# Kernel tuning notes

Hardware: AMD Instinct MI355X
Metric: run time of the kernel (lower is better)

Reference implementation:

```python
import jax, jax.numpy as jnp
import numpy as np

SHAPES = [(100, 100), (50, 50), (25, 25), (13, 13)]
N_HEADS, N_LEVELS, N_POINTS, D_MODEL, D_FFN = 8, 4, 4, 256, 1024
HEAD_DIM = D_MODEL // N_HEADS
S_TOTAL = sum(h * w for h, w in SHAPES)
BATCH = 2


def _layernorm(x, g, b, eps=1e-5):
    m = jnp.mean(x, -1, keepdims=True)
    v = jnp.mean((x - m) ** 2, -1, keepdims=True)
    return (x - m) * jax.lax.rsqrt(v + eps) * g + b


def _bilinear_sample(value_l, loc, Hl, Wl):
    # value_l: (N, Hl, Wl, nh, hd); loc: (N, Lq, nh, P, 2) normalized to [0,1]
    # Matches torch grid_sample(mode='bilinear', padding_mode='zeros', align_corners=False)
    x = loc[..., 0] * Wl - 0.5
    y = loc[..., 1] * Hl - 0.5
    x0 = jnp.floor(x); y0 = jnp.floor(y)
    wx1 = x - x0; wx0 = 1.0 - wx1
    wy1 = y - y0; wy0 = 1.0 - wy1
    x0i = x0.astype(jnp.int32); x1i = x0i + 1
    y0i = y0.astype(jnp.int32); y1i = y0i + 1
    N, Lq, nh, P = x.shape
    n_idx = jnp.arange(N)[:, None, None, None]
    h_idx = jnp.arange(nh)[None, None, :, None]

    def gather(yi, xi):
        valid = (yi >= 0) & (yi < Hl) & (xi >= 0) & (xi < Wl)
        yc = jnp.clip(yi, 0, Hl - 1); xc = jnp.clip(xi, 0, Wl - 1)
        v = value_l[n_idx, yc, xc, h_idx]  # (N, Lq, nh, P, hd)
        return v * valid[..., None].astype(v.dtype)

    return (gather(y0i, x0i) * (wy0 * wx0)[..., None]
            + gather(y0i, x1i) * (wy0 * wx1)[..., None]
            + gather(y1i, x0i) * (wy1 * wx0)[..., None]
            + gather(y1i, x1i) * (wy1 * wx1)[..., None])


def _forward(src, pos, reference_points, W_off, b_off, W_attn, b_attn, W_val, b_val,
             W_out, b_out, W1, b1, W2, b2, g1, beta1, g2, beta2):
    N, S, C = src.shape
    q = src + pos  # with_pos_embed
    # MSDeformAttn
    off = (q @ W_off + b_off).reshape(N, S, N_HEADS, N_LEVELS, N_POINTS, 2)
    aw = jax.nn.softmax((q @ W_attn + b_attn).reshape(N, S, N_HEADS, N_LEVELS * N_POINTS), axis=-1)
    aw = aw.reshape(N, S, N_HEADS, N_LEVELS, N_POINTS)
    value = (src @ W_val + b_val).reshape(N, S, N_HEADS, HEAD_DIM)
    # offset normalizer is (W_l, H_l) per level
    normalizer = jnp.array([[wl, hl] for hl, wl in SHAPES], dtype=src.dtype)  # (L, 2)
    loc = reference_points[:, :, None, :, None, :] + off / normalizer[None, None, None, :, None, :]
    out = jnp.zeros((N, S, N_HEADS, HEAD_DIM), src.dtype)
    start = 0
    for l, (Hl, Wl) in enumerate(SHAPES):
        v_l = value[:, start:start + Hl * Wl].reshape(N, Hl, Wl, N_HEADS, HEAD_DIM)
        sampled = _bilinear_sample(v_l, loc[:, :, :, l], Hl, Wl)  # (N,S,nh,P,hd)
        out = out + jnp.einsum('nqhp,nqhpd->nqhd', aw[:, :, :, l], sampled)
        start += Hl * Wl
    src2 = out.reshape(N, S, C) @ W_out + b_out
    # residual + norm1 (dropout is identity in eval)
    x = _layernorm(src + src2, g1, beta1)
    # FFN + residual + norm2
    ff = jax.nn.relu(x @ W1 + b1) @ W2 + b2
    return _layernorm(x + ff, g2, beta2)


def setup_inputs() -> dict:
    key = jax.random.key(0)
    ks = jax.random.split(key, 16)
    f32 = jnp.float32

    def w(k, shape, scale=0.02):
        return jax.random.normal(k, shape, dtype=f32) * scale

    return {
        "src": jax.random.normal(ks[0], (BATCH, S_TOTAL, D_MODEL), dtype=f32),
        "pos": jax.random.normal(ks[1], (BATCH, S_TOTAL, D_MODEL), dtype=f32),
        "reference_points": jax.random.uniform(ks[2], (BATCH, S_TOTAL, N_LEVELS, 2), dtype=f32),
        "spatial_shapes": jnp.array(SHAPES, dtype=jnp.int32),
        "level_start_index": jnp.array(np.cumsum([0] + [h * w for h, w in SHAPES[:-1]]), dtype=jnp.int32),
        "W_off": w(ks[3], (D_MODEL, N_HEADS * N_LEVELS * N_POINTS * 2)),
        "b_off": w(ks[4], (N_HEADS * N_LEVELS * N_POINTS * 2,), 0.5),
        "W_attn": w(ks[5], (D_MODEL, N_HEADS * N_LEVELS * N_POINTS)),
        "b_attn": w(ks[6], (N_HEADS * N_LEVELS * N_POINTS,)),
        "W_val": w(ks[7], (D_MODEL, D_MODEL)),
        "b_val": w(ks[8], (D_MODEL,)),
        "W_out": w(ks[9], (D_MODEL, D_MODEL)),
        "b_out": w(ks[10], (D_MODEL,)),
        "W1": w(ks[11], (D_MODEL, D_FFN)),
        "b1": w(ks[12], (D_FFN,)),
        "W2": w(ks[13], (D_FFN, D_MODEL)),
        "b2": w(ks[14], (D_MODEL,)),
        "g1": jnp.ones((D_MODEL,), f32),
        "beta1": jnp.zeros((D_MODEL,), f32),
        "g2": jnp.ones((D_MODEL,), f32),
        "beta2": jnp.zeros((D_MODEL,), f32),
    }


def reference(src, pos, reference_points, spatial_shapes, level_start_index,
              W_off, b_off, W_attn, b_attn, W_val, b_val, W_out, b_out,
              W1, b1, W2, b2, g1, beta1, g2, beta2):
    # spatial_shapes / level_start_index are static metadata mirrored by SHAPES
    return _forward(src, pos, reference_points, W_off, b_off, W_attn, b_attn,
                    W_val, b_val, W_out, b_out, W1, b1, W2, b2, g1, beta1, g2, beta2)
```

## Files before the change

### kernel.cpp

```cpp
#include <hip/hip_runtime.h>


typedef __bf16 bf16x8 __attribute__((ext_vector_type(8)));
typedef __bf16 bf16x4 __attribute__((ext_vector_type(4)));
typedef float floatx4 __attribute__((ext_vector_type(4)));

#define S_TOTAL 13294
#define M_ROWS  26588
#define M_PAD   26624

#define MFMA16(a, b, c) __builtin_amdgcn_mfma_f32_16x16x32_bf16(a, b, c, 0, 0, 0)

__global__ __launch_bounds__(256) void cvt_k(
    const float* __restrict__ Woff, const float* __restrict__ Wattn,
    const float* __restrict__ Wval, const float* __restrict__ Wout,
    const float* __restrict__ W1,   const float* __restrict__ W2,
    const float* __restrict__ boff, const float* __restrict__ battn,
    __bf16* __restrict__ wbase, float* __restrict__ bc) {
    int b = blockIdx.x;
    if (b >= 184) {
        for (int i = threadIdx.x; i < 384; i += 256)
            bc[i] = (i < 256) ? boff[i] : battn[i - 256];
        return;
    }
    const float* W; __bf16* D; int K, N, t;
    if (b < 16)       { W = Woff;  D = wbase;          K = 256;  N = 256;  t = b; }
    else if (b < 24)  { W = Wattn; D = wbase + 65536;  K = 256;  N = 128;  t = b - 16; }
    else if (b < 40)  { W = Wval;  D = wbase + 98304;  K = 256;  N = 256;  t = b - 24; }
    else if (b < 56)  { W = Wout;  D = wbase + 163840; K = 256;  N = 256;  t = b - 40; }
    else if (b < 120) { W = W1;    D = wbase + 229376; K = 256;  N = 1024; t = b - 56; }
    else              { W = W2;    D = wbase + 491520; K = 1024; N = 256;  t = b - 120; }
    int tk = K >> 6;
    int n0 = (t / tk) << 6, k0 = (t % tk) << 6;
    __shared__ float T[64][65];
    int tid = threadIdx.x;
    int rr = tid >> 4, cc = (tid & 15) << 2;
#pragma unroll
    for (int p = 0; p < 4; p++) {
        int r = p * 16 + rr;
        float4 v = *(const float4*)(W + (size_t)(k0 + r) * N + n0 + cc);
        T[r][cc] = v.x; T[r][cc + 1] = v.y; T[r][cc + 2] = v.z; T[r][cc + 3] = v.w;
    }
    __syncthreads();
#pragma unroll
    for (int p = 0; p < 4; p++) {
        int n = p * 16 + rr;
        bf16x4 o = {(__bf16)T[cc][n], (__bf16)T[cc + 1][n],
                    (__bf16)T[cc + 2][n], (__bf16)T[cc + 3][n]};
        *(bf16x4*)(D + (size_t)(n0 + n) * K + k0 + cc) = o;
    }
}

template <int J, bool SUMPOS, bool BF16OUT>
__global__ __launch_bounds__(512, 4) void gemm_src(
    const float* __restrict__ Af, const float* __restrict__ Pf,
    const __bf16* __restrict__ BT, const float* __restrict__ bias,
    float* __restrict__ Cf, __bf16* __restrict__ Cb, int N) {
    constexpr int ASTR = 264;
    __shared__ __align__(16) __bf16 As[64 * ASTR];
    __shared__ __align__(16) float patch[8][16 * 20];
    const int tid = threadIdx.x, wave = tid >> 6, lane = tid & 63;
    const int l16 = lane & 15, quad = lane >> 4;
    const int row0 = blockIdx.x * 64;
#pragma unroll
    for (int p = 0; p < 8; p++) {
        int fe = (p * 512 + tid) * 4;
        int m = fe >> 8, k = fe & 255;
        int row = min(row0 + m, M_ROWS - 1);
        float4 s = *(const float4*)(Af + (size_t)row * 256 + k);
        if (SUMPOS) {
            float4 pp = *(const float4*)(Pf + (size_t)row * 256 + k);
            s.x += pp.x; s.y += pp.y; s.z += pp.z; s.w += pp.w;
        }
        bf16x4 v = {(__bf16)s.x, (__bf16)s.y, (__bf16)s.z, (__bf16)s.w};
        *(bf16x4*)(As + m * ASTR + k) = v;
    }
    __syncthreads();
    const int n0 = wave * (J * 16);
    floatx4 acc[4][J] = {};
#pragma unroll
    for (int ki = 0; ki < 8; ki++) {
        bf16x8 af[4], bfr[J];
#pragma unroll
        for (int i = 0; i < 4; i++)
            af[i] = *(const bf16x8*)(As + (i * 16 + l16) * ASTR + ki * 32 + quad * 8);
#pragma unroll
        for (int j = 0; j < J; j++)
            bfr[j] = *(const bf16x8*)(BT + (size_t)(n0 + j * 16 + l16) * 256 + ki * 32 + quad * 8);
#pragma unroll
        for (int i = 0; i < 4; i++)
#pragma unroll
            for (int j = 0; j < J; j++)
                acc[i][j] = MFMA16(af[i], bfr[j], acc[i][j]);
    }
    float* pat = patch[wave];
    const int prow = lane >> 2, pc = lane & 3;
#pragma unroll
    for (int i = 0; i < 4; i++)
#pragma unroll
        for (int j = 0; j < J; j++) {
            float bv = bias[n0 + j * 16 + l16];
#pragma unroll
            for (int r = 0; r < 4; r++)
                pat[(quad * 4 + r) * 20 + l16] = acc[i][j][r] + bv;
            float4 v4 = *(float4*)&pat[prow * 20 + pc * 4];
            size_t gi = (size_t)(row0 + i * 16 + prow) * N + n0 + j * 16 + pc * 4;
            if (BF16OUT) {
                bf16x4 ob = {(__bf16)v4.x, (__bf16)v4.y, (__bf16)v4.z, (__bf16)v4.w};
                *(bf16x4*)(Cb + gi) = ob;
            } else {
                *(float4*)(Cf + gi) = v4;
            }
        }
}

__global__ __launch_bounds__(256) void sample_k(const float* __restrict__ offa,
                                                const __bf16* __restrict__ valb,
                                                const float* __restrict__ refp,
                                                __bf16* __restrict__ outb) {
    const int r   = blockIdx.x;
    const int tid = threadIdx.x;
    if (r >= M_ROWS) {
        outb[(size_t)r * 256 + tid] = (__bf16)0.f;
        return;
    }
    __shared__ float2 s_wo[4][128];
    const int n = (r >= S_TOTAL) ? 1 : 0;

    if (tid < 128) {
        const int HLc[4] = {100, 50, 25, 13};
        const int STc[4] = {0, 10000, 12500, 13125};
        int lp = tid & 15, l = lp >> 2;
        float logit = offa[(size_t)r * 384 + 256 + tid];
        float mx = logit;
        mx = fmaxf(mx, __shfl_xor(mx, 1));
        mx = fmaxf(mx, __shfl_xor(mx, 2));
        mx = fmaxf(mx, __shfl_xor(mx, 4));
        mx = fmaxf(mx, __shfl_xor(mx, 8));
        float e = __expf(logit - mx);
        float s = e;
        s += __shfl_xor(s, 1); s += __shfl_xor(s, 2);
        s += __shfl_xor(s, 4); s += __shfl_xor(s, 8);
        float aw = e / s;

        float2 o2 = *(const float2*)(offa + (size_t)r * 384 + tid * 2);
        float rx = refp[((size_t)r * 4 + l) * 2];
        float ry = refp[((size_t)r * 4 + l) * 2 + 1];
        int   Wl = HLc[l];
        float x = rx * (float)Wl + o2.x - 0.5f;
        float y = ry * (float)Wl + o2.y - 0.5f;
        float xf = floorf(x), yf = floorf(y);
        float wx1 = x - xf, wy1 = y - yf;
        float wx0 = 1.f - wx1, wy0 = 1.f - wy1;
        int x0 = (int)xf, y0 = (int)yf;
        int base = n * S_TOTAL + STc[l];
#pragma unroll
        for (int c = 0; c < 4; c++) {
            int yy = y0 + (c >> 1), xx = x0 + (c & 1);
            bool valid = (yy >= 0) & (yy < Wl) & (xx >= 0) & (xx < Wl);
            int yc = min(max(yy, 0), Wl - 1);
            int xc = min(max(xx, 0), Wl - 1);
            float w = ((c >> 1) ? wy1 : wy0) * ((c & 1) ? wx1 : wx0);
            int off = (base + yc * Wl + xc) * 512;
            s_wo[c][tid] = make_float2(valid ? w * aw : 0.f, __int_as_float(off));
        }
    }
    __syncthreads();

    const int h  = tid >> 5;
    const int pg = (tid >> 2) & 7;
    const int cg = tid & 3;
    const char* vbase = (const char*)valb + h * 64 + cg * 16;
    float a[8] = {};
#pragma unroll
    for (int pp = 0; pp < 2; pp++) {
        int idx = h * 16 + pg * 2 + pp;
#pragma unroll
        for (int c = 0; c < 4; c++) {
            float2 wo = s_wo[c][idx];
            float  w  = wo.x;
            bf16x8 v  = *(const bf16x8*)(vbase + __float_as_int(wo.y));
#pragma unroll
            for (int k = 0; k < 8; k++) a[k] += w * (float)v[k];
        }
    }
#pragma unroll
    for (int k = 0; k < 8; k++) {
        a[k] += __shfl_xor(a[k], 4);
        a[k] += __shfl_xor(a[k], 8);
        a[k] += __shfl_xor(a[k], 16);
    }
    if (pg == 0) {
        bf16x8 res;
#pragma unroll
        for (int k = 0; k < 8; k++) res[k] = (__bf16)a[k];
        *(bf16x8*)(outb + (size_t)r * 256 + h * 32 + cg * 8) = res;
    }
}

__global__ __launch_bounds__(512, 4) void oln_k(
    const __bf16* __restrict__ A, const __bf16* __restrict__ BT,
    const float* __restrict__ bias, const float* __restrict__ src,
    const float* __restrict__ g, const float* __restrict__ be,
    float* __restrict__ x, __bf16* __restrict__ xb) {
    constexpr int ASTR = 264;
    __shared__ __align__(16) __bf16 As[64 * ASTR];
    __shared__ __align__(16) float patch[8][16 * 20];
    __shared__ float2 rowred[64][9];
    const int tid = threadIdx.x, wave = tid >> 6, lane = tid & 63;
    const int l16 = lane & 15, quad = lane >> 4;
    const int prow = lane >> 2, pc = lane & 3;
    const int row0 = blockIdx.x * 64;
#pragma unroll
    for (int p = 0; p < 4; p++) {
        int fg = p * 512 + tid;
        int m = fg >> 5, gg = fg & 31;
        bf16x8 v = *(const bf16x8*)(A + (size_t)(row0 + m) * 256 + gg * 8);
        *(bf16x8*)(As + m * ASTR + gg * 8) = v;
    }
    __syncthreads();
    const int n0 = wave * 32;
    floatx4 acc[4][2] = {};
#pragma unroll
    for (int ki = 0; ki < 8; ki++) {
        bf16x8 af[4], bfr[2];
#pragma unroll
        for (int i = 0; i < 4; i++)
            af[i] = *(const bf16x8*)(As + (i * 16 + l16) * ASTR + ki * 32 + quad * 8);
#pragma unroll
        for (int j = 0; j < 2; j++)
            bfr[j] = *(const bf16x8*)(BT + (size_t)(n0 + j * 16 + l16) * 256 + ki * 32 + quad * 8);
#pragma unroll
        for (int i = 0; i < 4; i++)
#pragma unroll
            for (int j = 0; j < 2; j++)
                acc[i][j] = MFMA16(af[i], bfr[j], acc[i][j]);
    }
    float* pat = patch[wave];
    floatx4 v4[4][2];
#pragma unroll
    for (int i = 0; i < 4; i++) {
        int rowc = min(row0 + i * 16 + prow, M_ROWS - 1);
        float s_par = 0.f, q_par = 0.f;
#pragma unroll
        for (int j = 0; j < 2; j++) {
            float bv = bias[n0 + j * 16 + l16];
#pragma unroll
            for (int r = 0; r < 4; r++)
                pat[(quad * 4 + r) * 20 + l16] = acc[i][j][r] + bv;
            float4 t4 = *(float4*)&pat[prow * 20 + pc * 4];
            float4 r4 = *(const float4*)(src + (size_t)rowc * 256 + n0 + j * 16 + pc * 4);
            floatx4 w; w[0] = t4.x + r4.x; w[1] = t4.y + r4.y;
            w[2] = t4.z + r4.z; w[3] = t4.w + r4.w;
            v4[i][j] = w;
            s_par += w[0] + w[1] + w[2] + w[3];
            q_par += w[0] * w[0] + w[1] * w[1] + w[2] * w[2] + w[3] * w[3];
        }
        s_par += __shfl_xor(s_par, 1); s_par += __shfl_xor(s_par, 2);
        q_par += __shfl_xor(q_par, 1); q_par += __shfl_xor(q_par, 2);
        if (pc == 0) rowred[i * 16 + prow][wave] = make_float2(s_par, q_par);
    }
    __syncthreads();
#pragma unroll
    for (int i = 0; i < 4; i++) {
        float ss = 0.f, qq = 0.f;
#pragma unroll
        for (int w8 = 0; w8 < 8; w8++) {
            float2 t = rowred[i * 16 + prow][w8];
            ss += t.x; qq += t.y;
        }
        float mean = ss * (1.f / 256.f);
        float var  = qq * (1.f / 256.f) - mean * mean;
        float rstd = rsqrtf(var + 1e-5f);
#pragma unroll
        for (int j = 0; j < 2; j++) {
            int col = n0 + j * 16 + pc * 4;
            float4 g4 = *(const float4*)(g + col);
            float4 b4 = *(const float4*)(be + col);
            floatx4 w = v4[i][j];
            float4 o4;
            o4.x = (w[0] - mean) * rstd * g4.x + b4.x;
            o4.y = (w[1] - mean) * rstd * g4.y + b4.y;
            o4.z = (w[2] - mean) * rstd * g4.z + b4.z;
            o4.w = (w[3] - mean) * rstd * g4.w + b4.w;
            size_t gi = (size_t)(row0 + i * 16 + prow) * 256 + col;
            *(float4*)(x + gi) = o4;
            bf16x4 ob = {(__bf16)o4.x, (__bf16)o4.y, (__bf16)o4.z, (__bf16)o4.w};
            *(bf16x4*)(xb + gi) = ob;
        }
    }
}

__global__ __launch_bounds__(512, 4) void ffn_k(
    const __bf16* __restrict__ xb, const __bf16* __restrict__ W1T,
    const __bf16* __restrict__ W2T, const float* __restrict__ b1,
    const float* __restrict__ b2, const float* __restrict__ x,
    const float* __restrict__ g, const float* __restrict__ be,
    float* __restrict__ out) {
    constexpr int ASTR = 264, HSTR = 520;
    __shared__ __align__(16) __bf16 As[32 * ASTR];
    __shared__ __align__(16) __bf16 Hs[32 * HSTR];
    __shared__ __align__(16) float patch[8][16 * 20];
    __shared__ float2 rowred[32][9];
    const int tid = threadIdx.x, wave = tid >> 6, lane = tid & 63;
    const int l16 = lane & 15, quad = lane >> 4;
    const int prow = lane >> 2, pc = lane & 3;
    const int row0 = blockIdx.x * 32;
    float* pat = patch[wave];
#pragma unroll
    for (int p = 0; p < 2; p++) {
        int fg = p * 512 + tid;
        int m = fg >> 5, gg = fg & 31;
        bf16x8 v = *(const bf16x8*)(xb + (size_t)(row0 + m) * 256 + gg * 8);
        *(bf16x8*)(As + m * ASTR + gg * 8) = v;
    }
    __syncthreads();
    floatx4 facc[2][2] = {};
    for (int hc = 0; hc < 2; hc++) {
        floatx4 hacc[2][4] = {};
#pragma unroll
        for (int ki = 0; ki < 8; ki++) {
            bf16x8 af[2], bfr[4];
#pragma unroll
            for (int i = 0; i < 2; i++)
                af[i] = *(const bf16x8*)(As + (i * 16 + l16) * ASTR + ki * 32 + quad * 8);
#pragma unroll
            for (int j = 0; j < 4; j++) {
                int nn = hc * 512 + wave * 64 + j * 16 + l16;
                bfr[j] = *(const bf16x8*)(W1T + (size_t)nn * 256 + ki * 32 + quad * 8);
            }
#pragma unroll
            for (int i = 0; i < 2; i++)
#pragma unroll
                for (int j = 0; j < 4; j++)
                    hacc[i][j] = MFMA16(af[i], bfr[j], hacc[i][j]);
        }
#pragma unroll
        for (int i = 0; i < 2; i++)
#pragma unroll
            for (int j = 0; j < 4; j++) {
                float bv = b1[hc * 512 + wave * 64 + j * 16 + l16];
#pragma unroll
                for (int r = 0; r < 4; r++)
                    pat[(quad * 4 + r) * 20 + l16] = fmaxf(hacc[i][j][r] + bv, 0.f);
                float4 t4 = *(float4*)&pat[prow * 20 + pc * 4];
                bf16x4 h4 = {(__bf16)t4.x, (__bf16)t4.y, (__bf16)t4.z, (__bf16)t4.w};
                *(bf16x4*)(Hs + (i * 16 + prow) * HSTR + wave * 64 + j * 16 + pc * 4) = h4;
            }
        __syncthreads();
#pragma unroll
        for (int ki = 0; ki < 16; ki++) {
            bf16x8 ah[2], bfr[2];
#pragma unroll
            for (int i = 0; i < 2; i++)
                ah[i] = *(const bf16x8*)(Hs + (i * 16 + l16) * HSTR + ki * 32 + quad * 8);
#pragma unroll
            for (int j = 0; j < 2; j++) {
                int nn = wave * 32 + j * 16 + l16;
                bfr[j] = *(const bf16x8*)(W2T + (size_t)nn * 1024 + hc * 512 + ki * 32 + quad * 8);
            }
#pragma unroll
            for (int i = 0; i < 2; i++)
#pragma unroll
                for (int j = 0; j < 2; j++)
                    facc[i][j] = MFMA16(ah[i], bfr[j], facc[i][j]);
        }
        __syncthreads();
    }
    const int n0 = wave * 32;
    floatx4 v4[2][2];
#pragma unroll
    for (int i = 0; i < 2; i++) {
        int rowi = row0 + i * 16 + prow;
        float s_par = 0.f, q_par = 0.f;
#pragma unroll
        for (int j = 0; j < 2; j++) {
            float bv = b2[n0 + j * 16 + l16];
#pragma unroll
            for (int r = 0; r < 4; r++)
                pat[(quad * 4 + r) * 20 + l16] = facc[i][j][r] + bv;
            float4 t4 = *(float4*)&pat[prow * 20 + pc * 4];
            float4 r4 = *(const float4*)(x + (size_t)rowi * 256 + n0 + j * 16 + pc * 4);
            floatx4 w; w[0] = t4.x + r4.x; w[1] = t4.y + r4.y;
            w[2] = t4.z + r4.z; w[3] = t4.w + r4.w;
            v4[i][j] = w;
            s_par += w[0] + w[1] + w[2] + w[3];
            q_par += w[0] * w[0] + w[1] * w[1] + w[2] * w[2] + w[3] * w[3];
        }
        s_par += __shfl_xor(s_par, 1); s_par += __shfl_xor(s_par, 2);
        q_par += __shfl_xor(q_par, 1); q_par += __shfl_xor(q_par, 2);
        if (pc == 0) rowred[i * 16 + prow][wave] = make_float2(s_par, q_par);
    }
    __syncthreads();
#pragma unroll
    for (int i = 0; i < 2; i++) {
        float ss = 0.f, qq = 0.f;
#pragma unroll
        for (int w8 = 0; w8 < 8; w8++) {
            float2 t = rowred[i * 16 + prow][w8];
            ss += t.x; qq += t.y;
        }
        float mean = ss * (1.f / 256.f);
        float var  = qq * (1.f / 256.f) - mean * mean;
        float rstd = rsqrtf(var + 1e-5f);
        int row = row0 + i * 16 + prow;
        if (row < M_ROWS) {
#pragma unroll
            for (int j = 0; j < 2; j++) {
                int col = n0 + j * 16 + pc * 4;
                float4 g4 = *(const float4*)(g + col);
                float4 b4 = *(const float4*)(be + col);
                floatx4 w = v4[i][j];
                float4 o4;
                o4.x = (w[0] - mean) * rstd * g4.x + b4.x;
                o4.y = (w[1] - mean) * rstd * g4.y + b4.y;
                o4.z = (w[2] - mean) * rstd * g4.z + b4.z;
                o4.w = (w[3] - mean) * rstd * g4.w + b4.w;
                *(float4*)(out + (size_t)row * 256 + col) = o4;
            }
        }
    }
}

extern "C" void kernel_launch(void* const* d_in, const int* in_sizes, int n_in,
                              void* d_out, int out_size, void* d_ws, size_t ws_size,
                              hipStream_t stream) {
    const float* src  = (const float*)d_in[0];
    const float* pos  = (const float*)d_in[1];
    const float* refp = (const float*)d_in[2];
    const float* W_off  = (const float*)d_in[5];
    const float* b_off  = (const float*)d_in[6];
    const float* W_attn = (const float*)d_in[7];
    const float* b_attn = (const float*)d_in[8];
    const float* W_val  = (const float*)d_in[9];
    const float* b_val  = (const float*)d_in[10];
    const float* W_out  = (const float*)d_in[11];
    const float* b_out  = (const float*)d_in[12];
    const float* W1     = (const float*)d_in[13];
    const float* b1     = (const float*)d_in[14];
    const float* W2     = (const float*)d_in[15];
    const float* b2     = (const float*)d_in[16];
    const float* g1     = (const float*)d_in[17];
    const float* beta1  = (const float*)d_in[18];
    const float* g2     = (const float*)d_in[19];
    const float* beta2  = (const float*)d_in[20];
    float* out = (float*)d_out;

    const size_t RB = (size_t)M_PAD * 256 * 2;
    const size_t RF = (size_t)M_PAD * 256 * 4;
    char* ws = (char*)d_ws;
    __bf16* outb = (__bf16*)(ws);
    __bf16* valb = (__bf16*)(ws + RB);
    float*  offa = (float*)(ws + 2 * RB);
    float*  x    = (float*)(ws + 2 * RB);
    __bf16* xb   = (__bf16*)(ws + 2 * RB + RF);
    char*   regW = ws + 2 * RB + (size_t)M_PAD * 384 * 4;

    __bf16* WTcomb = (__bf16*)regW;
    __bf16* WTval  = (__bf16*)(regW + 196608);
    __bf16* WTout  = (__bf16*)(regW + 327680);
    __bf16* WT1    = (__bf16*)(regW + 458752);
    __bf16* WT2    = (__bf16*)(regW + 983040);
    float*  bc     = (float*)(regW + 1507328);

    cvt_k<<<185, 256, 0, stream>>>(W_off, W_attn, W_val, W_out, W1, W2,
                                   b_off, b_attn, WTcomb, bc);

    gemm_src<3, true, false><<<416, 512, 0, stream>>>(
        src, pos, WTcomb, bc, offa, nullptr, 384);
    gemm_src<2, false, true><<<416, 512, 0, stream>>>(
        src, src, WTval, b_val, nullptr, valb, 256);

    sample_k<<<M_PAD, 256, 0, stream>>>(offa, valb, refp, outb);

    oln_k<<<416, 512, 0, stream>>>(outb, WTout, b_out, src, g1, beta1, x, xb);

    ffn_k<<<832, 512, 0, stream>>>(xb, WT1, WT2, b1, b2, x, g2, beta2, out);
}
```

Measured before the change: 362.7 us.

## Halve GEMM row tiles, double-buffer weight loads, drop LDS patch epilogues

The gemm_src and oln_k kernels now use 32-row tiles with twice as many blocks, and every GEMM loop including FFN prefetches the next k-slice of weight fragments into registers. The LDS transpose patch epilogues are replaced by direct scalar stores from the MFMA accumulator layout. LayerNorm row sums are reduced with wave shuffles plus LDS atomics instead of a per-wave table. The FFN hidden dimension is processed in four 256-wide chunks to shrink the Hs buffer. This aims to raise occupancy and hide global weight-load latency, at the cost of uncoalesced scalar stores and more weight re-reads across blocks.

```diff
diff --git a/kernel.cpp b/kernel.cpp
--- a/kernel.cpp
+++ b/kernel.cpp
@@ -57,13 +57,12 @@
     const __bf16* __restrict__ BT, const float* __restrict__ bias,
     float* __restrict__ Cf, __bf16* __restrict__ Cb, int N) {
     constexpr int ASTR = 264;
-    __shared__ __align__(16) __bf16 As[64 * ASTR];
-    __shared__ __align__(16) float patch[8][16 * 20];
+    __shared__ __align__(16) __bf16 As[32 * ASTR];
     const int tid = threadIdx.x, wave = tid >> 6, lane = tid & 63;
     const int l16 = lane & 15, quad = lane >> 4;
-    const int row0 = blockIdx.x * 64;
-#pragma unroll
-    for (int p = 0; p < 8; p++) {
+    const int row0 = blockIdx.x * 32;
+#pragma unroll
+    for (int p = 0; p < 4; p++) {
         int fe = (p * 512 + tid) * 4;
         int m = fe >> 8, k = fe & 255;
         int row = min(row0 + m, M_ROWS - 1);
@@ -77,41 +76,44 @@
     }
     __syncthreads();
     const int n0 = wave * (J * 16);
-    floatx4 acc[4][J] = {};
+    floatx4 acc[2][J] = {};
+    bf16x8 bb[2][J];
+#pragma unroll
+    for (int j = 0; j < J; j++)
+        bb[0][j] = *(const bf16x8*)(BT + (size_t)(n0 + j * 16 + l16) * 256 + quad * 8);
 #pragma unroll
     for (int ki = 0; ki < 8; ki++) {
-        bf16x8 af[4], bfr[J];
-#pragma unroll
-        for (int i = 0; i < 4; i++)
+        const int cur = ki & 1;
+        if (ki < 7) {
+#pragma unroll
+            for (int j = 0; j < J; j++)
+                bb[cur ^ 1][j] = *(const bf16x8*)(BT + (size_t)(n0 + j * 16 + l16) * 256
+                                                  + (ki + 1) * 32 + quad * 8);
+        }
+        bf16x8 af[2];
+#pragma unroll
+        for (int i = 0; i < 2; i++)
             af[i] = *(const bf16x8*)(As + (i * 16 + l16) * ASTR + ki * 32 + quad * 8);
 #pragma unroll
+        for (int i = 0; i < 2; i++)
+#pragma unroll
+            for (int j = 0; j < J; j++)
+                acc[i][j] = MFMA16(af[i], bb[cur][j], acc[i][j]);
+    }
+    float bv[J];
+#pragma unroll
+    for (int j = 0; j < J; j++) bv[j] = bias[n0 + j * 16 + l16];
+#pragma unroll
+    for (int i = 0; i < 2; i++)
+#pragma unroll
         for (int j = 0; j < J; j++)
-            bfr[j] = *(const bf16x8*)(BT + (size_t)(n0 + j * 16 + l16) * 256 + ki * 32 + quad * 8);
-#pragma unroll
-        for (int i = 0; i < 4; i++)
-#pragma unroll
-            for (int j = 0; j < J; j++)
-                acc[i][j] = MFMA16(af[i], bfr[j], acc[i][j]);
-    }
-    float* pat = patch[wave];
-    const int prow = lane >> 2, pc = lane & 3;
-#pragma unroll
-    for (int i = 0; i < 4; i++)
-#pragma unroll
-        for (int j = 0; j < J; j++) {
-            float bv = bias[n0 + j * 16 + l16];
-#pragma unroll
-            for (int r = 0; r < 4; r++)
-                pat[(quad * 4 + r) * 20 + l16] = acc[i][j][r] + bv;
-            float4 v4 = *(float4*)&pat[prow * 20 + pc * 4];
-            size_t gi = (size_t)(row0 + i * 16 + prow) * N + n0 + j * 16 + pc * 4;
-            if (BF16OUT) {
-                bf16x4 ob = {(__bf16)v4.x, (__bf16)v4.y, (__bf16)v4.z, (__bf16)v4.w};
-                *(bf16x4*)(Cb + gi) = ob;
-            } else {
-                *(float4*)(Cf + gi) = v4;
-            }
-        }
+#pragma unroll
+            for (int r = 0; r < 4; r++) {
+                float v = acc[i][j][r] + bv[j];
+                size_t gi = (size_t)(row0 + i * 16 + quad * 4 + r) * N + n0 + j * 16 + l16;
+                if (BF16OUT) Cb[gi] = (__bf16)v;
+                else         Cf[gi] = v;
+            }
 }
 
 __global__ __launch_bounds__(256) void sample_k(const float* __restrict__ offa,
@@ -204,91 +206,90 @@
     const float* __restrict__ g, const float* __restrict__ be,
     float* __restrict__ x, __bf16* __restrict__ xb) {
     constexpr int ASTR = 264;
-    __shared__ __align__(16) __bf16 As[64 * ASTR];
-    __shared__ __align__(16) float patch[8][16 * 20];
-    __shared__ float2 rowred[64][9];
+    __shared__ __align__(16) __bf16 As[32 * ASTR];
+    __shared__ float rs[32], rq[32];
     const int tid = threadIdx.x, wave = tid >> 6, lane = tid & 63;
     const int l16 = lane & 15, quad = lane >> 4;
-    const int prow = lane >> 2, pc = lane & 3;
-    const int row0 = blockIdx.x * 64;
-#pragma unroll
-    for (int p = 0; p < 4; p++) {
+    const int row0 = blockIdx.x * 32;
+#pragma unroll
+    for (int p = 0; p < 2; p++) {
         int fg = p * 512 + tid;
         int m = fg >> 5, gg = fg & 31;
-        bf16x8 v = *(const bf16x8*)(A + (size_t)(row0 + m) * 256 + gg * 8);
-        *(bf16x8*)(As + m * ASTR + gg * 8) = v;
-    }
+        *(bf16x8*)(As + m * ASTR + gg * 8) =
+            *(const bf16x8*)(A + (size_t)(row0 + m) * 256 + gg * 8);
+    }
+    if (tid < 32) { rs[tid] = 0.f; rq[tid] = 0.f; }
     __syncthreads();
     const int n0 = wave * 32;
-    floatx4 acc[4][2] = {};
+    floatx4 acc[2][2] = {};
+    bf16x8 bb[2][2];
+#pragma unroll
+    for (int j = 0; j < 2; j++)
+        bb[0][j] = *(const bf16x8*)(BT + (size_t)(n0 + j * 16 + l16) * 256 + quad * 8);
 #pragma unroll
     for (int ki = 0; ki < 8; ki++) {
-        bf16x8 af[4], bfr[2];
-#pragma unroll
-        for (int i = 0; i < 4; i++)
+        const int cur = ki & 1;
+        if (ki < 7) {
+#pragma unroll
+            for (int j = 0; j < 2; j++)
+                bb[cur ^ 1][j] = *(const bf16x8*)(BT + (size_t)(n0 + j * 16 + l16) * 256
+                                                  + (ki + 1) * 32 + quad * 8);
+        }
+        bf16x8 af[2];
+#pragma unroll
+        for (int i = 0; i < 2; i++)
             af[i] = *(const bf16x8*)(As + (i * 16 + l16) * ASTR + ki * 32 + quad * 8);
 #pragma unroll
-        for (int j = 0; j < 2; j++)
-            bfr[j] = *(const bf16x8*)(BT + (size_t)(n0 + j * 16 + l16) * 256 + ki * 32 + quad * 8);
-#pragma unroll
-        for (int i = 0; i < 4; i++)
+        for (int i = 0; i < 2; i++)
 #pragma unroll
             for (int j = 0; j < 2; j++)
-                acc[i][j] = MFMA16(af[i], bfr[j], acc[i][j]);
-    }
-    float* pat = patch[wave];
-    floatx4 v4[4][2];
-#pragma unroll
-    for (int i = 0; i < 4; i++) {
-        int rowc = min(row0 + i * 16 + prow, M_ROWS - 1);
-        float s_par = 0.f, q_par = 0.f;
-#pragma unroll
-        for (int j = 0; j < 2; j++) {
-            float bv = bias[n0 + j * 16 + l16];
-#pragma unroll
-            for (int r = 0; r < 4; r++)
-                pat[(quad * 4 + r) * 20 + l16] = acc[i][j][r] + bv;
-            float4 t4 = *(float4*)&pat[prow * 20 + pc * 4];
-            float4 r4 = *(const float4*)(src + (size_t)rowc * 256 + n0 + j * 16 + pc * 4);
-            floatx4 w; w[0] = t4.x + r4.x; w[1] = t4.y + r4.y;
-            w[2] = t4.z + r4.z; w[3] = t4.w + r4.w;
-            v4[i][j] = w;
-            s_par += w[0] + w[1] + w[2] + w[3];
-            q_par += w[0] * w[0] + w[1] * w[1] + w[2] * w[2] + w[3] * w[3];
-        }
-        s_par += __shfl_xor(s_par, 1); s_par += __shfl_xor(s_par, 2);
-        q_par += __shfl_xor(q_par, 1); q_par += __shfl_xor(q_par, 2);
-        if (pc == 0) rowred[i * 16 + prow][wave] = make_float2(s_par, q_par);
-    }
-    __syncthreads();
-#pragma unroll
-    for (int i = 0; i < 4; i++) {
-        float ss = 0.f, qq = 0.f;
-#pragma unroll
-        for (int w8 = 0; w8 < 8; w8++) {
-            float2 t = rowred[i * 16 + prow][w8];
-            ss += t.x; qq += t.y;
-        }
-        float mean = ss * (1.f / 256.f);
-        float var  = qq * (1.f / 256.f) - mean * mean;
-        float rstd = rsqrtf(var + 1e-5f);
-#pragma unroll
-        for (int j = 0; j < 2; j++) {
-            int col = n0 + j * 16 + pc * 4;
-            float4 g4 = *(const float4*)(g + col);
-            float4 b4 = *(const float4*)(be + col);
-            floatx4 w = v4[i][j];
-            float4 o4;
-            o4.x = (w[0] - mean) * rstd * g4.x + b4.x;
-            o4.y = (w[1] - mean) * rstd * g4.y + b4.y;
-            o4.z = (w[2] - mean) * rstd * g4.z + b4.z;
-            o4.w = (w[3] - mean) * rstd * g4.w + b4.w;
-            size_t gi = (size_t)(row0 + i * 16 + prow) * 256 + col;
-            *(float4*)(x + gi) = o4;
-            bf16x4 ob = {(__bf16)o4.x, (__bf16)o4.y, (__bf16)o4.z, (__bf16)o4.w};
-            *(bf16x4*)(xb + gi) = ob;
-        }
-    }
+                acc[i][j] = MFMA16(af[i], bb[cur][j], acc[i][j]);
+    }
+    float bv[2], gv[2], bev[2];
+#pragma unroll
+    for (int j = 0; j < 2; j++) {
+        bv[j]  = bias[n0 + j * 16 + l16];
+        gv[j]  = g[n0 + j * 16 + l16];
+        bev[j] = be[n0 + j * 16 + l16];
+    }
+    float vals[2][2][4];
+#pragma unroll
+    for (int i = 0; i < 2; i++)
+#pragma unroll
+        for (int r = 0; r < 4; r++) {
+            int lrow = i * 16 + quad * 4 + r;
+            int rowc = min(row0 + lrow, M_ROWS - 1);
+            float s = 0.f, q = 0.f;
+#pragma unroll
+            for (int j = 0; j < 2; j++) {
+                float v = acc[i][j][r] + bv[j]
+                        + src[(size_t)rowc * 256 + n0 + j * 16 + l16];
+                vals[i][j][r] = v;
+                s += v; q += v * v;
+            }
+            s += __shfl_xor(s, 1); s += __shfl_xor(s, 2);
+            s += __shfl_xor(s, 4); s += __shfl_xor(s, 8);
+            q += __shfl_xor(q, 1); q += __shfl_xor(q, 2);
+            q += __shfl_xor(q, 4); q += __shfl_xor(q, 8);
+            if (l16 == 0) { atomicAdd(&rs[lrow], s); atomicAdd(&rq[lrow], q); }
+        }
+    __syncthreads();
+#pragma unroll
+    for (int i = 0; i < 2; i++)
+#pragma unroll
+        for (int r = 0; r < 4; r++) {
+            int lrow = i * 16 + quad * 4 + r;
+            float mean = rs[lrow] * (1.f / 256.f);
+            float var  = rq[lrow] * (1.f / 256.f) - mean * mean;
+            float rstd = rsqrtf(var + 1e-5f);
+#pragma unroll
+            for (int j = 0; j < 2; j++) {
+                float o = (vals[i][j][r] - mean) * rstd * gv[j] + bev[j];
+                size_t gi = (size_t)(row0 + lrow) * 256 + n0 + j * 16 + l16;
+                x[gi]  = o;
+                xb[gi] = (__bf16)o;
+            }
+        }
 }
 
 __global__ __launch_bounds__(512, 4) void ffn_k(
@@ -297,129 +298,145 @@
     const float* __restrict__ b2, const float* __restrict__ x,
     const float* __restrict__ g, const float* __restrict__ be,
     float* __restrict__ out) {
-    constexpr int ASTR = 264, HSTR = 520;
+    constexpr int ASTR = 264, HSTR = 264;
     __shared__ __align__(16) __bf16 As[32 * ASTR];
     __shared__ __align__(16) __bf16 Hs[32 * HSTR];
-    __shared__ __align__(16) float patch[8][16 * 20];
-    __shared__ float2 rowred[32][9];
+    __shared__ float rs[32], rq[32];
     const int tid = threadIdx.x, wave = tid >> 6, lane = tid & 63;
     const int l16 = lane & 15, quad = lane >> 4;
-    const int prow = lane >> 2, pc = lane & 3;
     const int row0 = blockIdx.x * 32;
-    float* pat = patch[wave];
 #pragma unroll
     for (int p = 0; p < 2; p++) {
         int fg = p * 512 + tid;
         int m = fg >> 5, gg = fg & 31;
-        bf16x8 v = *(const bf16x8*)(xb + (size_t)(row0 + m) * 256 + gg * 8);
-        *(bf16x8*)(As + m * ASTR + gg * 8) = v;
-    }
-    __syncthreads();
+        *(bf16x8*)(As + m * ASTR + gg * 8) =
+            *(const bf16x8*)(xb + (size_t)(row0 + m) * 256 + gg * 8);
+    }
+    if (tid < 32) { rs[tid] = 0.f; rq[tid] = 0.f; }
+    __syncthreads();
+
+    float b1v[4][2];
+#pragma unroll
+    for (int hc = 0; hc < 4; hc++)
+#pragma unroll
+        for (int j = 0; j < 2; j++)
+            b1v[hc][j] = b1[hc * 256 + wave * 32 + j * 16 + l16];
+
     floatx4 facc[2][2] = {};
-    for (int hc = 0; hc < 2; hc++) {
-        floatx4 hacc[2][4] = {};
-#pragma unroll
-        for (int ki = 0; ki < 8; ki++) {
-            bf16x8 af[2], bfr[4];
-#pragma unroll
-            for (int i = 0; i < 2; i++)
-                af[i] = *(const bf16x8*)(As + (i * 16 + l16) * ASTR + ki * 32 + quad * 8);
-#pragma unroll
-            for (int j = 0; j < 4; j++) {
-                int nn = hc * 512 + wave * 64 + j * 16 + l16;
-                bfr[j] = *(const bf16x8*)(W1T + (size_t)nn * 256 + ki * 32 + quad * 8);
-            }
-#pragma unroll
-            for (int i = 0; i < 2; i++)
-#pragma unroll
-                for (int j = 0; j < 4; j++)
-                    hacc[i][j] = MFMA16(af[i], bfr[j], hacc[i][j]);
-        }
+#pragma unroll
+    for (int hc = 0; hc < 4; hc++) {
+        floatx4 hacc[2][2] = {};
+        {
+            bf16x8 wb[2][2];
+#pragma unroll
+            for (int j = 0; j < 2; j++)
+                wb[0][j] = *(const bf16x8*)(W1T
+                    + (size_t)(hc * 256 + wave * 32 + j * 16 + l16) * 256 + quad * 8);
+#pragma unroll
+            for (int ki = 0; ki < 8; ki++) {
+                const int cur = ki & 1;
+                if (ki < 7) {
+#pragma unroll
+                    for (int j = 0; j < 2; j++)
+                        wb[cur ^ 1][j] = *(const bf16x8*)(W1T
+                            + (size_t)(hc * 256 + wave * 32 + j * 16 + l16) * 256
+                            + (ki + 1) * 32 + quad * 8);
+                }
+                bf16x8 af[2];
+#pragma unroll
+                for (int i = 0; i < 2; i++)
+                    af[i] = *(const bf16x8*)(As + (i * 16 + l16) * ASTR + ki * 32 + quad * 8);
+#pragma unroll
+                for (int i = 0; i < 2; i++)
+#pragma unroll
+                    for (int j = 0; j < 2; j++)
+                        hacc[i][j] = MFMA16(af[i], wb[cur][j], hacc[i][j]);
+            }
+        }
+        __syncthreads();
 #pragma unroll
         for (int i = 0; i < 2; i++)
 #pragma unroll
-            for (int j = 0; j < 4; j++) {
-                float bv = b1[hc * 512 + wave * 64 + j * 16 + l16];
+            for (int j = 0; j < 2; j++)
 #pragma unroll
                 for (int r = 0; r < 4; r++)
-                    pat[(quad * 4 + r) * 20 + l16] = fmaxf(hacc[i][j][r] + bv, 0.f);
-                float4 t4 = *(float4*)&pat[prow * 20 + pc * 4];
-                bf16x4 h4 = {(__bf16)t4.x, (__bf16)t4.y, (__bf16)t4.z, (__bf16)t4.w};
-                *(bf16x4*)(Hs + (i * 16 + prow) * HSTR + wave * 64 + j * 16 + pc * 4) = h4;
-            }
+                    Hs[(i * 16 + quad * 4 + r) * HSTR + wave * 32 + j * 16 + l16] =
+                        (__bf16)fmaxf(hacc[i][j][r] + b1v[hc][j], 0.f);
         __syncthreads();
-#pragma unroll
-        for (int ki = 0; ki < 16; ki++) {
-            bf16x8 ah[2], bfr[2];
-#pragma unroll
-            for (int i = 0; i < 2; i++)
-                ah[i] = *(const bf16x8*)(Hs + (i * 16 + l16) * HSTR + ki * 32 + quad * 8);
+        {
+            bf16x8 wb[2][2];
+#pragma unroll
+            for (int j = 0; j < 2; j++)
+                wb[0][j] = *(const bf16x8*)(W2T
+                    + (size_t)(wave * 32 + j * 16 + l16) * 1024 + hc * 256 + quad * 8);
+#pragma unroll
+            for (int ki = 0; ki < 8; ki++) {
+                const int cur = ki & 1;
+                if (ki < 7) {
+#pragma unroll
+                    for (int j = 0; j < 2; j++)
+                        wb[cur ^ 1][j] = *(const bf16x8*)(W2T
+                            + (size_t)(wave * 32 + j * 16 + l16) * 1024
+                            + hc * 256 + (ki + 1) * 32 + quad * 8);
+                }
+                bf16x8 ah[2];
+#pragma unroll
+                for (int i = 0; i < 2; i++)
+                    ah[i] = *(const bf16x8*)(Hs + (i * 16 + l16) * HSTR + ki * 32 + quad * 8);
+#pragma unroll
+                for (int i = 0; i < 2; i++)
+#pragma unroll
+                    for (int j = 0; j < 2; j++)
+                        facc[i][j] = MFMA16(ah[i], wb[cur][j], facc[i][j]);
+            }
+        }
+    }
+    const int n0 = wave * 32;
+    float b2v[2], gv[2], bev[2];
+#pragma unroll
+    for (int j = 0; j < 2; j++) {
+        b2v[j] = b2[n0 + j * 16 + l16];
+        gv[j]  = g[n0 + j * 16 + l16];
+        bev[j] = be[n0 + j * 16 + l16];
+    }
+    float vals[2][2][4];
+#pragma unroll
+    for (int i = 0; i < 2; i++)
+#pragma unroll
+        for (int r = 0; r < 4; r++) {
+            int lrow = i * 16 + quad * 4 + r;
+            float s = 0.f, q = 0.f;
 #pragma unroll
             for (int j = 0; j < 2; j++) {
-                int nn = wave * 32 + j * 16 + l16;
-                bfr[j] = *(const bf16x8*)(W2T + (size_t)nn * 1024 + hc * 512 + ki * 32 + quad * 8);
-            }
-#pragma unroll
-            for (int i = 0; i < 2; i++)
-#pragma unroll
-                for (int j = 0; j < 2; j++)
-                    facc[i][j] = MFMA16(ah[i], bfr[j], facc[i][j]);
-        }
-        __syncthreads();
-    }
-    const int n0 = wave * 32;
-    floatx4 v4[2][2];
-#pragma unroll
-    for (int i = 0; i < 2; i++) {
-        int rowi = row0 + i * 16 + prow;
-        float s_par = 0.f, q_par = 0.f;
-#pragma unroll
-        for (int j = 0; j < 2; j++) {
-            float bv = b2[n0 + j * 16 + l16];
-#pragma unroll
-            for (int r = 0; r < 4; r++)
-                pat[(quad * 4 + r) * 20 + l16] = facc[i][j][r] + bv;
-            float4 t4 = *(float4*)&pat[prow * 20 + pc * 4];
-            float4 r4 = *(const float4*)(x + (size_t)rowi * 256 + n0 + j * 16 + pc * 4);
-            floatx4 w; w[0] = t4.x + r4.x; w[1] = t4.y + r4.y;
-            w[2] = t4.z + r4.z; w[3] = t4.w + r4.w;
-            v4[i][j] = w;
-            s_par += w[0] + w[1] + w[2] + w[3];
-            q_par += w[0] * w[0] + w[1] * w[1] + w[2] * w[2] + w[3] * w[3];
-        }
-        s_par += __shfl_xor(s_par, 1); s_par += __shfl_xor(s_par, 2);
-        q_par += __shfl_xor(q_par, 1); q_par += __shfl_xor(q_par, 2);
-        if (pc == 0) rowred[i * 16 + prow][wave] = make_float2(s_par, q_par);
-    }
-    __syncthreads();
-#pragma unroll
-    for (int i = 0; i < 2; i++) {
-        float ss = 0.f, qq = 0.f;
-#pragma unroll
-        for (int w8 = 0; w8 < 8; w8++) {
-            float2 t = rowred[i * 16 + prow][w8];
-            ss += t.x; qq += t.y;
-        }
-        float mean = ss * (1.f / 256.f);
-        float var  = qq * (1.f / 256.f) - mean * mean;
-        float rstd = rsqrtf(var + 1e-5f);
-        int row = row0 + i * 16 + prow;
-        if (row < M_ROWS) {
-#pragma unroll
-            for (int j = 0; j < 2; j++) {
-                int col = n0 + j * 16 + pc * 4;
-                float4 g4 = *(const float4*)(g + col);
-                float4 b4 = *(const float4*)(be + col);
-                floatx4 w = v4[i][j];
-                float4 o4;
-                o4.x = (w[0] - mean) * rstd * g4.x + b4.x;
-                o4.y = (w[1] - mean) * rstd * g4.y + b4.y;
-                o4.z = (w[2] - mean) * rstd * g4.z + b4.z;
-                o4.w = (w[3] - mean) * rstd * g4.w + b4.w;
-                *(float4*)(out + (size_t)row * 256 + col) = o4;
-            }
-        }
-    }
+                float v = facc[i][j][r] + b2v[j]
+                        + x[(size_t)(row0 + lrow) * 256 + n0 + j * 16 + l16];
+                vals[i][j][r] = v;
+                s += v; q += v * v;
+            }
+            s += __shfl_xor(s, 1); s += __shfl_xor(s, 2);
+            s += __shfl_xor(s, 4); s += __shfl_xor(s, 8);
+            q += __shfl_xor(q, 1); q += __shfl_xor(q, 2);
+            q += __shfl_xor(q, 4); q += __shfl_xor(q, 8);
+            if (l16 == 0) { atomicAdd(&rs[lrow], s); atomicAdd(&rq[lrow], q); }
+        }
+    __syncthreads();
+#pragma unroll
+    for (int i = 0; i < 2; i++)
+#pragma unroll
+        for (int r = 0; r < 4; r++) {
+            int lrow = i * 16 + quad * 4 + r;
+            int row  = row0 + lrow;
+            if (row < M_ROWS) {
+                float mean = rs[lrow] * (1.f / 256.f);
+                float var  = rq[lrow] * (1.f / 256.f) - mean * mean;
+                float rstd = rsqrtf(var + 1e-5f);
+#pragma unroll
+                for (int j = 0; j < 2; j++) {
+                    float o = (vals[i][j][r] - mean) * rstd * gv[j] + bev[j];
+                    out[(size_t)row * 256 + n0 + j * 16 + l16] = o;
+                }
+            }
+        }
 }
 
 extern "C" void kernel_launch(void* const* d_in, const int* in_sizes, int n_in,
@@ -466,14 +483,14 @@
     cvt_k<<<185, 256, 0, stream>>>(W_off, W_attn, W_val, W_out, W1, W2,
                                    b_off, b_attn, WTcomb, bc);
 
-    gemm_src<3, true, false><<<416, 512, 0, stream>>>(
+    gemm_src<3, true, false><<<832, 512, 0, stream>>>(
         src, pos, WTcomb, bc, offa, nullptr, 384);
-    gemm_src<2, false, true><<<416, 512, 0, stream>>>(
+    gemm_src<2, false, true><<<832, 512, 0, stream>>>(
         src, src, WTval, b_val, nullptr, valb, 256);
 
     sample_k<<<M_PAD, 256, 0, stream>>>(offa, valb, refp, outb);
 
-    oln_k<<<416, 512, 0, stream>>>(outb, WTout, b_out, src, g1, beta1, x, xb);
+    oln_k<<<832, 512, 0, stream>>>(outb, WTout, b_out, src, g1, beta1, x, xb);
 
     ffn_k<<<832, 512, 0, stream>>>(xb, WT1, WT2, b1, b2, x, g2, beta2, out);
 }
```

New measurement: 390.6 us. +7.7%, slower.
